# Performance work log

Measured on AMD Instinct MI355X. Metric: run time of the kernel, lower is better.

## Reference

```python
import jax, jax.numpy as jnp
import numpy as np

N = 50000
E = 800000
F_IN = 128
HID = 128
NCLS = 40


def setup_inputs() -> dict:
    key = jax.random.key(0)
    ks = jax.random.split(key, 12)
    def glorot(k, fan_in, fan_out):
        s = jnp.sqrt(6.0 / (fan_in + fan_out))
        return jax.random.uniform(k, (fan_in, fan_out), jnp.float32, -s, s)
    x = jax.random.normal(ks[0], (N, F_IN), jnp.float32)
    edge_index = jax.random.randint(ks[1], (2, E), 0, N, jnp.int64)
    W1 = glorot(ks[2], F_IN, HID); b1 = jnp.zeros((HID,), jnp.float32)
    W2 = glorot(ks[3], HID, HID);  b2 = jnp.zeros((HID,), jnp.float32)
    W3 = glorot(ks[4], HID, HID);  b3 = jnp.zeros((HID,), jnp.float32)
    Wc = glorot(ks[5], HID, NCLS)
    bc = jnp.zeros((NCLS,), jnp.float32)
    return {"x": x, "edge_index": edge_index, "W1": W1, "b1": b1,
            "W2": W2, "b2": b2, "W3": W3, "b3": b3, "Wc": Wc, "bc": bc}


def _gcn_conv(h, src, dst, norm, W, b):
    # GCNConv: linear transform, then normalized scatter-add aggregation
    h = h @ W                              # [N, out]
    msg = h[src] * norm[:, None]           # [E+N, out] gathered + scaled
    out = jax.ops.segment_sum(msg, dst, num_segments=N)
    return out + b


def reference(x, edge_index, W1, b1, W2, b2, W3, b3, Wc, bc):
    # add self-loops (PyG GCNConv default) and compute symmetric norm once
    loop = jnp.arange(N, dtype=edge_index.dtype)
    src = jnp.concatenate([edge_index[0], loop])
    dst = jnp.concatenate([edge_index[1], loop])
    deg = jax.ops.segment_sum(jnp.ones_like(dst, dtype=x.dtype), dst, num_segments=N)
    dinv = jax.lax.rsqrt(deg)              # deg >= 1 due to self-loops
    norm = dinv[src] * dinv[dst]           # [E+N]

    h = jax.nn.relu(_gcn_conv(x, src, dst, norm, W1, b1))
    h = jax.nn.relu(_gcn_conv(h, src, dst, norm, W2, b2))
    h = jax.nn.relu(_gcn_conv(h, src, dst, norm, W3, b3))
    out = h @ Wc + bc
    return (out, h)
```

## Files before the change

### kernel.cpp

```cpp
#include <hip/hip_runtime.h>
#include <hip/hip_fp16.h>


#define FEAT 128

typedef _Float16 half_t;
typedef _Float16 f16x8 __attribute__((ext_vector_type(8)));
typedef float f32x16 __attribute__((ext_vector_type(16)));


__global__ __launch_bounds__(256) void k_prep(const float* __restrict__ W1,
                                              const float* __restrict__ W2,
                                              const float* __restrict__ W3,
                                              half_t* __restrict__ Wt1,
                                              half_t* __restrict__ Wt2,
                                              half_t* __restrict__ Wt3,
                                              int* __restrict__ deg, int N) {
  int idx = blockIdx.x * 256 + threadIdx.x;
  if (idx < N) deg[idx] = 0;
  if (idx < 3 * 16384) {
    int which = idx >> 14;
    int i = idx & 16383;
    int k = i >> 7, n = i & 127;
    const float* W = (which == 0) ? W1 : (which == 1) ? W2 : W3;
    half_t* Wt = (which == 0) ? Wt1 : (which == 1) ? Wt2 : Wt3;
    Wt[n * 128 + k] = (half_t)W[i];
  }
}


__global__ __launch_bounds__(256) void k_count_rank(const int* __restrict__ dst,
                                                    int* __restrict__ deg,
                                                    int* __restrict__ rank, int E) {
  int e = blockIdx.x * 256 + threadIdx.x;
  if (e < E) rank[e] = atomicAdd(&deg[dst[e]], 1);
}

__global__ __launch_bounds__(256) void k_scanA(const int* __restrict__ deg,
                                               int* __restrict__ partial, int N) {
  __shared__ int s[256];
  int t = threadIdx.x;
  int i = blockIdx.x * 256 + t;
  s[t] = (i < N) ? deg[i] : 0;
  __syncthreads();
  for (int off = 128; off > 0; off >>= 1) {
    if (t < off) s[t] += s[t + off];
    __syncthreads();
  }
  if (t == 0) partial[blockIdx.x] = s[0];
}

__global__ __launch_bounds__(256) void k_scanB(int* __restrict__ partial, int nblk,
                                               int* __restrict__ offsets, int N) {
  __shared__ int s[256];
  int t = threadIdx.x;
  int v = (t < nblk) ? partial[t] : 0;
  s[t] = v;
  __syncthreads();
  for (int off = 1; off < 256; off <<= 1) {
    int x = (t >= off) ? s[t - off] : 0;
    __syncthreads();
    s[t] += x;
    __syncthreads();
  }
  if (t < nblk) partial[t] = s[t] - v;
  if (t == 0) offsets[N] = s[255];
}

__global__ __launch_bounds__(256) void k_scanC(const int* __restrict__ deg,
                                               const int* __restrict__ partial,
                                               int* __restrict__ offsets,
                                               float* __restrict__ dinv, int N) {
  __shared__ int s[256];
  int t = threadIdx.x;
  int i = blockIdx.x * 256 + t;
  int v = (i < N) ? deg[i] : 0;
  s[t] = v;
  __syncthreads();
  for (int off = 1; off < 256; off <<= 1) {
    int x = (t >= off) ? s[t - off] : 0;
    __syncthreads();
    s[t] += x;
    __syncthreads();
  }
  if (i < N) {
    offsets[i] = partial[blockIdx.x] + s[t] - v;
    dinv[i] = rsqrtf((float)(v + 1));
  }
}

__global__ __launch_bounds__(256) void k_place(const int* __restrict__ src,
                                               const int* __restrict__ dst,
                                               const int* __restrict__ offsets,
                                               const int* __restrict__ rank,
                                               int* __restrict__ col, int E) {
  int e = blockIdx.x * 256 + threadIdx.x;
  if (e < E) col[offsets[dst[e]] + rank[e]] = src[e];
}

template <int SRC_FP32>
__global__ __launch_bounds__(256) void k_gemm_mfma(const void* __restrict__ Asrc,
                                                   const half_t* __restrict__ Wt,
                                                   const float* __restrict__ dinv,
                                                   half_t* __restrict__ T,
                                                   int nrows) {
  __shared__ char lds[65536];
  char* sA = lds;
  char* sW = lds + 32768;
  int t = threadIdx.x;
  int rowBase = blockIdx.x * 128;
  int rowsHere = min(128, nrows - rowBase);

  #pragma unroll
  for (int i = 0; i < 8; ++i) {
    int lin = t + i * 256;
    int r = lin >> 4, c = lin & 15;
    *(float4*)(sW + r * 256 + ((c * 16) ^ ((r & 15) << 4))) =
        *(const float4*)((const char*)Wt + r * 256 + c * 16);
  }
  if (SRC_FP32) {
    const float* Af = (const float*)Asrc;
    #pragma unroll
    for (int i = 0; i < 8; ++i) {
      int lin = t + i * 256;
      int r = lin >> 4, c = lin & 15;
      f16x8 h = {};
      if (r < rowsHere) {
        const float4* p = (const float4*)(Af + (size_t)(rowBase + r) * FEAT + c * 8);
        float4 v0 = p[0], v1 = p[1];
        h[0] = (half_t)v0.x; h[1] = (half_t)v0.y; h[2] = (half_t)v0.z; h[3] = (half_t)v0.w;
        h[4] = (half_t)v1.x; h[5] = (half_t)v1.y; h[6] = (half_t)v1.z; h[7] = (half_t)v1.w;
      }
      *(f16x8*)(sA + r * 256 + ((c * 16) ^ ((r & 15) << 4))) = h;
    }
  } else {
    const char* Ah = (const char*)Asrc;
    #pragma unroll
    for (int i = 0; i < 8; ++i) {
      int lin = t + i * 256;
      int r = lin >> 4, c = lin & 15;
      float4 v = {};
      if (r < rowsHere) v = *(const float4*)(Ah + (size_t)(rowBase + r) * 256 + c * 16);
      *(float4*)(sA + r * 256 + ((c * 16) ^ ((r & 15) << 4))) = v;
    }
  }
  __syncthreads();

  int wv = t >> 6;
  int l = t & 63;
  int l31 = l & 31;
  int lhi = l >> 5;
  int sw = (l31 & 15) << 4;

  f32x16 acc[4] = {};

  #pragma unroll
  for (int step = 0; step < 8; ++step) {
    int ko = (step * 32 + lhi * 16) ^ sw;
    f16x8 a  = *(const f16x8*)(sA + (wv * 32 + l31) * 256 + ko);
    f16x8 b0 = *(const f16x8*)(sW + (l31) * 256 + ko);
    f16x8 b1 = *(const f16x8*)(sW + (32 + l31) * 256 + ko);
    f16x8 b2 = *(const f16x8*)(sW + (64 + l31) * 256 + ko);
    f16x8 b3 = *(const f16x8*)(sW + (96 + l31) * 256 + ko);
    acc[0] = __builtin_amdgcn_mfma_f32_32x32x16_f16(a, b0, acc[0], 0, 0, 0);
    acc[1] = __builtin_amdgcn_mfma_f32_32x32x16_f16(a, b1, acc[1], 0, 0, 0);
    acc[2] = __builtin_amdgcn_mfma_f32_32x32x16_f16(a, b2, acc[2], 0, 0, 0);
    acc[3] = __builtin_amdgcn_mfma_f32_32x32x16_f16(a, b3, acc[3], 0, 0, 0);
  }

  #pragma unroll
  for (int j = 0; j < 16; ++j) {
    int rloc = wv * 32 + (j & 3) + 8 * (j >> 2) + 4 * lhi;
    if (rloc < rowsHere) {
      int grow = rowBase + rloc;
      float d = dinv[grow];
      #pragma unroll
      for (int n = 0; n < 4; ++n) {
        T[(size_t)grow * FEAT + n * 32 + l31] = (half_t)(acc[n][j] * d);
      }
    }
  }
}

template <int OUTF>
__global__ __launch_bounds__(256) void k_aggregate(const uint2* __restrict__ T4,
                                                   const int* __restrict__ offsets,
                                                   const int* __restrict__ col,
                                                   const float* __restrict__ dinv,
                                                   const float* __restrict__ bias,
                                                   float4* __restrict__ outF,
                                                   uint2* __restrict__ outH,
                                                   int N) {
  int wave = threadIdx.x >> 6;
  int half = (threadIdx.x >> 5) & 1;
  int q = threadIdx.x & 31;
  int node = (blockIdx.x * 4 + wave) * 2 + half;
  if (node >= N) return;
  int e0 = offsets[node], e1 = offsets[node + 1];

  uint2 sv = T4[(size_t)node * 32 + q];
  __half2 h0 = *(__half2*)&sv.x, h1 = *(__half2*)&sv.y;
  float ax = __half2float(h0.x), ay = __half2float(h0.y);
  float az = __half2float(h1.x), aw = __half2float(h1.y);

  int e = e0;
  for (; e + 8 <= e1; e += 8) {
    int s0 = col[e + 0], s1 = col[e + 1], s2 = col[e + 2], s3 = col[e + 3];
    int s4 = col[e + 4], s5 = col[e + 5], s6 = col[e + 6], s7 = col[e + 7];
    uint2 v0 = T4[(size_t)s0 * 32 + q];
    uint2 v1 = T4[(size_t)s1 * 32 + q];
    uint2 v2 = T4[(size_t)s2 * 32 + q];
    uint2 v3 = T4[(size_t)s3 * 32 + q];
    uint2 v4 = T4[(size_t)s4 * 32 + q];
    uint2 v5 = T4[(size_t)s5 * 32 + q];
    uint2 v6 = T4[(size_t)s6 * 32 + q];
    uint2 v7 = T4[(size_t)s7 * 32 + q];
    #pragma unroll
    for (int u = 0; u < 8; ++u) {
      uint2 v = (u == 0) ? v0 : (u == 1) ? v1 : (u == 2) ? v2 : (u == 3) ? v3
              : (u == 4) ? v4 : (u == 5) ? v5 : (u == 6) ? v6 : v7;
      __half2 p0 = *(__half2*)&v.x, p1 = *(__half2*)&v.y;
      ax += __half2float(p0.x); ay += __half2float(p0.y);
      az += __half2float(p1.x); aw += __half2float(p1.y);
    }
  }
  for (; e < e1; ++e) {
    uint2 v = T4[(size_t)col[e] * 32 + q];
    __half2 p0 = *(__half2*)&v.x, p1 = *(__half2*)&v.y;
    ax += __half2float(p0.x); ay += __half2float(p0.y);
    az += __half2float(p1.x); aw += __half2float(p1.y);
  }

  float di = dinv[node];
  float4 b = ((const float4*)bias)[q];
  float ox = fmaxf(di * ax + b.x, 0.f);
  float oy = fmaxf(di * ay + b.y, 0.f);
  float oz = fmaxf(di * az + b.z, 0.f);
  float ow = fmaxf(di * aw + b.w, 0.f);
  if (OUTF) {
    outF[(size_t)node * 32 + q] = make_float4(ox, oy, oz, ow);
  } else {
    uint2 o;
    __half2 t0 = __floats2half2_rn(ox, oy), t1 = __floats2half2_rn(oz, ow);
    o.x = *(unsigned*)&t0; o.y = *(unsigned*)&t1;
    outH[(size_t)node * 32 + q] = o;
  }
}

__global__ __launch_bounds__(256) void k_classifier(const float* __restrict__ h,
                                                    const float* __restrict__ Wc,
                                                    const float* __restrict__ bc,
                                                    float* __restrict__ out, int N) {
  __shared__ float sh[64 * 132];
  __shared__ float sWt[40 * 130];
  int t = threadIdx.x;
  int nodeBase = blockIdx.x * 64;
  int nodesHere = min(64, N - nodeBase);

  for (int i = t; i < FEAT * 40; i += 256) {
    int k = i / 40, c = i - k * 40;
    sWt[c * 130 + k] = Wc[i];
  }
  {
    const float4* H4 = (const float4*)(h + (size_t)nodeBase * FEAT);
    #pragma unroll
    for (int i = 0; i < 8; ++i) {
      int lin = t + i * 256;
      int r = lin >> 5, kc = lin & 31;
      float4 v = make_float4(0.f, 0.f, 0.f, 0.f);
      if (r < nodesHere) v = H4[lin];
      *(float4*)&sh[r * 132 + kc * 4] = v;
    }
  }
  __syncthreads();

  int n0 = (t >> 3) * 2;
  int cg = (t & 7) * 5;
  float acc0[5], acc1[5];
  #pragma unroll
  for (int j = 0; j < 5; ++j) { acc0[j] = bc[cg + j]; acc1[j] = acc0[j]; }

  #pragma unroll 4
  for (int k4 = 0; k4 < 32; ++k4) {
    float4 h0 = *(const float4*)&sh[n0 * 132 + k4 * 4];
    float4 h1 = *(const float4*)&sh[(n0 + 1) * 132 + k4 * 4];
    #pragma unroll
    for (int j = 0; j < 5; ++j) {
      float4 w = *(const float4*)&sWt[(cg + j) * 130 + k4 * 4];
      acc0[j] += h0.x * w.x + h0.y * w.y + h0.z * w.z + h0.w * w.w;
      acc1[j] += h1.x * w.x + h1.y * w.y + h1.z * w.z + h1.w * w.w;
    }
  }

  if (n0 < nodesHere) {
    float* o = out + (size_t)(nodeBase + n0) * 40 + cg;
    #pragma unroll
    for (int j = 0; j < 5; ++j) o[j] = acc0[j];
  }
  if (n0 + 1 < nodesHere) {
    float* o = out + (size_t)(nodeBase + n0 + 1) * 40 + cg;
    #pragma unroll
    for (int j = 0; j < 5; ++j) o[j] = acc1[j];
  }
}


extern "C" void kernel_launch(void* const* d_in, const int* in_sizes, int n_in,
                              void* d_out, int out_size, void* d_ws, size_t ws_size,
                              hipStream_t stream) {
  const float* x    = (const float*)d_in[0];
  const int*   edge = (const int*)d_in[1];
  const float* W1   = (const float*)d_in[2];
  const float* b1   = (const float*)d_in[3];
  const float* W2   = (const float*)d_in[4];
  const float* b2   = (const float*)d_in[5];
  const float* W3   = (const float*)d_in[6];
  const float* b3   = (const float*)d_in[7];
  const float* Wc   = (const float*)d_in[8];
  const float* bc   = (const float*)d_in[9];

  int N = in_sizes[0] / FEAT;
  int E = in_sizes[1] / 2;

  float* out  = (float*)d_out;
  float* hOut = out + (size_t)N * 40;

  size_t o = 0;
  char* wsb = (char*)d_ws;
  auto take = [&](size_t bytes) -> void* {
    void* p = wsb + o;
    o += (bytes + 255) & ~(size_t)255;
    return p;
  };
  float*   dinv    = (float*)take((size_t)N * 4);
  int*     deg     = (int*)take((size_t)N * 4);
  int*     rank    = (int*)take((size_t)E * 4);
  int*     partial = (int*)take(256 * 4);
  int*     offsets = (int*)take(((size_t)N + 8) * 4);
  int*     col     = (int*)take((size_t)E * 4);
  half_t*  T2h     = (half_t*)take((size_t)N * FEAT * 2);
  half_t*  Bh      = (half_t*)take((size_t)N * FEAT * 2);
  half_t*  Wt1     = (half_t*)take(16384 * 2);
  half_t*  Wt2     = (half_t*)take(16384 * 2);
  half_t*  Wt3     = (half_t*)take(16384 * 2);

  const int* e_src = edge;
  const int* e_dst = edge + E;

  int nblk = (N + 255) / 256;
  int eblk = (E + 255) / 256;

  k_prep<<<nblk, 256, 0, stream>>>(W1, W2, W3, Wt1, Wt2, Wt3, deg, N);
  k_count_rank<<<eblk, 256, 0, stream>>>(e_dst, deg, rank, E);
  k_scanA<<<nblk, 256, 0, stream>>>(deg, partial, N);
  k_scanB<<<1, 256, 0, stream>>>(partial, nblk, offsets, N);
  k_scanC<<<nblk, 256, 0, stream>>>(deg, partial, offsets, dinv, N);
  k_place<<<eblk, 256, 0, stream>>>(e_src, e_dst, offsets, rank, col, E);

  int gblk = (N + 127) / 128;
  int ablk = (N + 7) / 8;
  uint2* T4 = (uint2*)T2h;
  k_gemm_mfma<1><<<gblk, 256, 0, stream>>>(x, Wt1, dinv, T2h, N);
  k_aggregate<0><<<ablk, 256, 0, stream>>>(T4, offsets, col, dinv, b1, nullptr,
                                           (uint2*)Bh, N);
  k_gemm_mfma<0><<<gblk, 256, 0, stream>>>(Bh, Wt2, dinv, T2h, N);
  k_aggregate<0><<<ablk, 256, 0, stream>>>(T4, offsets, col, dinv, b2, nullptr,
                                           (uint2*)Bh, N);
  k_gemm_mfma<0><<<gblk, 256, 0, stream>>>(Bh, Wt3, dinv, T2h, N);
  k_aggregate<1><<<ablk, 256, 0, stream>>>(T4, offsets, col, dinv, b3,
                                           (float4*)hOut, nullptr, N);
  k_classifier<<<(N + 63) / 64, 256, 0, stream>>>(hOut, Wc, bc, out, N);
}
```

Measured before the change: 230.3 us.

## Widen aggregate gathers, split GEMM weight staging, fold scan kernels, add nontemporal hints

The aggregation kernel now gives each lane 16-byte fp16 loads (8 features) with 16 lanes per node and 16 nodes per block, up from 8-byte loads and 32 lanes per node. This halves the number of gather instructions and doubles the memory-level parallelism per lane. The GEMM loads the weight tile in two 64-row halves, cutting LDS from 64KB to 48KB to allow higher occupancy, at the cost of an extra barrier. The single-block scan pass is removed: each block now serially sums the preceding partials itself, which is O(nblk) work per block but saves one launch. Nontemporal loads and stores are added to the rank, col, output and intermediate-feature streams.

After: 253.7 us. +10.1%, slower.

```diff
diff --git a/kernel.cpp b/kernel.cpp
--- a/kernel.cpp
+++ b/kernel.cpp
@@ -7,6 +7,7 @@
 typedef _Float16 half_t;
 typedef _Float16 f16x8 __attribute__((ext_vector_type(8)));
 typedef float f32x16 __attribute__((ext_vector_type(16)));
+typedef unsigned int u32x4 __attribute__((ext_vector_type(4)));
 
 
 __global__ __launch_bounds__(256) void k_prep(const float* __restrict__ W1,
@@ -33,7 +34,10 @@
                                                     int* __restrict__ deg,
                                                     int* __restrict__ rank, int E) {
   int e = blockIdx.x * 256 + threadIdx.x;
-  if (e < E) rank[e] = atomicAdd(&deg[dst[e]], 1);
+  if (e < E) {
+    int r = atomicAdd(&deg[dst[e]], 1);
+    __builtin_nontemporal_store(r, &rank[e]);
+  }
 }
 
 __global__ __launch_bounds__(256) void k_scanA(const int* __restrict__ deg,
@@ -50,30 +54,15 @@
   if (t == 0) partial[blockIdx.x] = s[0];
 }
 
-__global__ __launch_bounds__(256) void k_scanB(int* __restrict__ partial, int nblk,
-                                               int* __restrict__ offsets, int N) {
+__global__ __launch_bounds__(256) void k_scanC2(const int* __restrict__ deg,
+                                                const int* __restrict__ partial,
+                                                int* __restrict__ offsets,
+                                                float* __restrict__ dinv, int N) {
   __shared__ int s[256];
   int t = threadIdx.x;
-  int v = (t < nblk) ? partial[t] : 0;
-  s[t] = v;
-  __syncthreads();
-  for (int off = 1; off < 256; off <<= 1) {
-    int x = (t >= off) ? s[t - off] : 0;
-    __syncthreads();
-    s[t] += x;
-    __syncthreads();
-  }
-  if (t < nblk) partial[t] = s[t] - v;
-  if (t == 0) offsets[N] = s[255];
-}
-
-__global__ __launch_bounds__(256) void k_scanC(const int* __restrict__ deg,
-                                               const int* __restrict__ partial,
-                                               int* __restrict__ offsets,
-                                               float* __restrict__ dinv, int N) {
-  __shared__ int s[256];
-  int t = threadIdx.x;
   int i = blockIdx.x * 256 + t;
+  int base = 0;
+  for (int j = 0; j < blockIdx.x; ++j) base += partial[j];
   int v = (i < N) ? deg[i] : 0;
   s[t] = v;
   __syncthreads();
@@ -84,8 +73,9 @@
     __syncthreads();
   }
   if (i < N) {
-    offsets[i] = partial[blockIdx.x] + s[t] - v;
+    offsets[i] = base + s[t] - v;
     dinv[i] = rsqrtf((float)(v + 1));
+    if (i == N - 1) offsets[N] = base + s[t];
   }
 }
 
@@ -95,7 +85,10 @@
                                                const int* __restrict__ rank,
                                                int* __restrict__ col, int E) {
   int e = blockIdx.x * 256 + threadIdx.x;
-  if (e < E) col[offsets[dst[e]] + rank[e]] = src[e];
+  if (e < E) {
+    int r = __builtin_nontemporal_load(&rank[e]);
+    col[offsets[dst[e]] + r] = src[e];
+  }
 }
 
 template <int SRC_FP32>
@@ -104,20 +97,13 @@
                                                    const float* __restrict__ dinv,
                                                    half_t* __restrict__ T,
                                                    int nrows) {
-  __shared__ char lds[65536];
+  __shared__ char lds[49152];
   char* sA = lds;
   char* sW = lds + 32768;
   int t = threadIdx.x;
   int rowBase = blockIdx.x * 128;
   int rowsHere = min(128, nrows - rowBase);
 
-  #pragma unroll
-  for (int i = 0; i < 8; ++i) {
-    int lin = t + i * 256;
-    int r = lin >> 4, c = lin & 15;
-    *(float4*)(sW + r * 256 + ((c * 16) ^ ((r & 15) << 4))) =
-        *(const float4*)((const char*)Wt + r * 256 + c * 16);
-  }
   if (SRC_FP32) {
     const float* Af = (const float*)Asrc;
     #pragma unroll
@@ -144,7 +130,6 @@
       *(float4*)(sA + r * 256 + ((c * 16) ^ ((r & 15) << 4))) = v;
     }
   }
-  __syncthreads();
 
   int wv = t >> 6;
   int l = t & 63;
@@ -155,17 +140,25 @@
   f32x16 acc[4] = {};
 
   #pragma unroll
-  for (int step = 0; step < 8; ++step) {
-    int ko = (step * 32 + lhi * 16) ^ sw;
-    f16x8 a  = *(const f16x8*)(sA + (wv * 32 + l31) * 256 + ko);
-    f16x8 b0 = *(const f16x8*)(sW + (l31) * 256 + ko);
-    f16x8 b1 = *(const f16x8*)(sW + (32 + l31) * 256 + ko);
-    f16x8 b2 = *(const f16x8*)(sW + (64 + l31) * 256 + ko);
-    f16x8 b3 = *(const f16x8*)(sW + (96 + l31) * 256 + ko);
-    acc[0] = __builtin_amdgcn_mfma_f32_32x32x16_f16(a, b0, acc[0], 0, 0, 0);
-    acc[1] = __builtin_amdgcn_mfma_f32_32x32x16_f16(a, b1, acc[1], 0, 0, 0);
-    acc[2] = __builtin_amdgcn_mfma_f32_32x32x16_f16(a, b2, acc[2], 0, 0, 0);
-    acc[3] = __builtin_amdgcn_mfma_f32_32x32x16_f16(a, b3, acc[3], 0, 0, 0);
+  for (int ch = 0; ch < 2; ++ch) {
+    if (ch) __syncthreads();
+    #pragma unroll
+    for (int i = 0; i < 4; ++i) {
+      int lin = t + i * 256;
+      int r = lin >> 4, c = lin & 15;
+      *(float4*)(sW + r * 256 + ((c * 16) ^ ((r & 15) << 4))) =
+          *(const float4*)((const char*)Wt + (ch * 64 + r) * 256 + c * 16);
+    }
+    __syncthreads();
+    #pragma unroll
+    for (int step = 0; step < 8; ++step) {
+      int ko = (step * 32 + lhi * 16) ^ sw;
+      f16x8 a  = *(const f16x8*)(sA + (wv * 32 + l31) * 256 + ko);
+      f16x8 b0 = *(const f16x8*)(sW + (l31) * 256 + ko);
+      f16x8 b1 = *(const f16x8*)(sW + (32 + l31) * 256 + ko);
+      acc[2 * ch + 0] = __builtin_amdgcn_mfma_f32_32x32x16_f16(a, b0, acc[2 * ch + 0], 0, 0, 0);
+      acc[2 * ch + 1] = __builtin_amdgcn_mfma_f32_32x32x16_f16(a, b1, acc[2 * ch + 1], 0, 0, 0);
+    }
   }
 
   #pragma unroll
@@ -182,68 +175,88 @@
   }
 }
 
+
+__device__ __forceinline__ void acc8(float* a, u32x4 v) {
+  unsigned w0 = v[0], w1 = v[1], w2 = v[2], w3 = v[3];
+  __half2 p0 = *(__half2*)&w0, p1 = *(__half2*)&w1;
+  __half2 p2 = *(__half2*)&w2, p3 = *(__half2*)&w3;
+  a[0] += __half2float(p0.x); a[1] += __half2float(p0.y);
+  a[2] += __half2float(p1.x); a[3] += __half2float(p1.y);
+  a[4] += __half2float(p2.x); a[5] += __half2float(p2.y);
+  a[6] += __half2float(p3.x); a[7] += __half2float(p3.y);
+}
+
+__device__ __forceinline__ void gather_node(const u32x4* __restrict__ T8,
+                                            const int* __restrict__ offsets,
+                                            const int* __restrict__ col,
+                                            int node, int q, float* a) {
+  u32x4 sv = T8[(size_t)node * 16 + q];
+  {
+    unsigned w0 = sv[0], w1 = sv[1], w2 = sv[2], w3 = sv[3];
+    __half2 p0 = *(__half2*)&w0, p1 = *(__half2*)&w1;
+    __half2 p2 = *(__half2*)&w2, p3 = *(__half2*)&w3;
+    a[0] = __half2float(p0.x); a[1] = __half2float(p0.y);
+    a[2] = __half2float(p1.x); a[3] = __half2float(p1.y);
+    a[4] = __half2float(p2.x); a[5] = __half2float(p2.y);
+    a[6] = __half2float(p3.x); a[7] = __half2float(p3.y);
+  }
+  int e0 = offsets[node], e1 = offsets[node + 1];
+  int e = e0;
+  for (; e + 8 <= e1; e += 8) {
+    int s[8];
+    u32x4 v[8];
+    #pragma unroll
+    for (int u = 0; u < 8; ++u) s[u] = __builtin_nontemporal_load(&col[e + u]);
+    #pragma unroll
+    for (int u = 0; u < 8; ++u) v[u] = T8[(size_t)s[u] * 16 + q];
+    #pragma unroll
+    for (int u = 0; u < 8; ++u) acc8(a, v[u]);
+  }
+  for (; e < e1; ++e) {
+    int s = __builtin_nontemporal_load(&col[e]);
+    acc8(a, T8[(size_t)s * 16 + q]);
+  }
+}
+
 template <int OUTF>
-__global__ __launch_bounds__(256) void k_aggregate(const uint2* __restrict__ T4,
+__global__ __launch_bounds__(256) void k_aggregate(const u32x4* __restrict__ T8,
                                                    const int* __restrict__ offsets,
                                                    const int* __restrict__ col,
                                                    const float* __restrict__ dinv,
                                                    const float* __restrict__ bias,
+                                                   u32x4* __restrict__ outH,
                                                    float4* __restrict__ outF,
-                                                   uint2* __restrict__ outH,
                                                    int N) {
-  int wave = threadIdx.x >> 6;
-  int half = (threadIdx.x >> 5) & 1;
-  int q = threadIdx.x & 31;
-  int node = (blockIdx.x * 4 + wave) * 2 + half;
+  int t = threadIdx.x;
+  int node = blockIdx.x * 16 + (t >> 4);
+  int q = t & 15;
   if (node >= N) return;
-  int e0 = offsets[node], e1 = offsets[node + 1];
-
-  uint2 sv = T4[(size_t)node * 32 + q];
-  __half2 h0 = *(__half2*)&sv.x, h1 = *(__half2*)&sv.y;
-  float ax = __half2float(h0.x), ay = __half2float(h0.y);
-  float az = __half2float(h1.x), aw = __half2float(h1.y);
-
-  int e = e0;
-  for (; e + 8 <= e1; e += 8) {
-    int s0 = col[e + 0], s1 = col[e + 1], s2 = col[e + 2], s3 = col[e + 3];
-    int s4 = col[e + 4], s5 = col[e + 5], s6 = col[e + 6], s7 = col[e + 7];
-    uint2 v0 = T4[(size_t)s0 * 32 + q];
-    uint2 v1 = T4[(size_t)s1 * 32 + q];
-    uint2 v2 = T4[(size_t)s2 * 32 + q];
-    uint2 v3 = T4[(size_t)s3 * 32 + q];
-    uint2 v4 = T4[(size_t)s4 * 32 + q];
-    uint2 v5 = T4[(size_t)s5 * 32 + q];
-    uint2 v6 = T4[(size_t)s6 * 32 + q];
-    uint2 v7 = T4[(size_t)s7 * 32 + q];
-    #pragma unroll
-    for (int u = 0; u < 8; ++u) {
-      uint2 v = (u == 0) ? v0 : (u == 1) ? v1 : (u == 2) ? v2 : (u == 3) ? v3
-              : (u == 4) ? v4 : (u == 5) ? v5 : (u == 6) ? v6 : v7;
-      __half2 p0 = *(__half2*)&v.x, p1 = *(__half2*)&v.y;
-      ax += __half2float(p0.x); ay += __half2float(p0.y);
-      az += __half2float(p1.x); aw += __half2float(p1.y);
-    }
-  }
-  for (; e < e1; ++e) {
-    uint2 v = T4[(size_t)col[e] * 32 + q];
-    __half2 p0 = *(__half2*)&v.x, p1 = *(__half2*)&v.y;
-    ax += __half2float(p0.x); ay += __half2float(p0.y);
-    az += __half2float(p1.x); aw += __half2float(p1.y);
-  }
+
+  float a[8];
+  gather_node(T8, offsets, col, node, q, a);
 
   float di = dinv[node];
-  float4 b = ((const float4*)bias)[q];
-  float ox = fmaxf(di * ax + b.x, 0.f);
-  float oy = fmaxf(di * ay + b.y, 0.f);
-  float oz = fmaxf(di * az + b.z, 0.f);
-  float ow = fmaxf(di * aw + b.w, 0.f);
+  const float4* b4 = (const float4*)bias;
+  float4 bA = b4[2 * q], bB = b4[2 * q + 1];
+  float o0 = fmaxf(di * a[0] + bA.x, 0.f);
+  float o1 = fmaxf(di * a[1] + bA.y, 0.f);
+  float o2 = fmaxf(di * a[2] + bA.z, 0.f);
+  float o3 = fmaxf(di * a[3] + bA.w, 0.f);
+  float o4 = fmaxf(di * a[4] + bB.x, 0.f);
+  float o5 = fmaxf(di * a[5] + bB.y, 0.f);
+  float o6 = fmaxf(di * a[6] + bB.z, 0.f);
+  float o7 = fmaxf(di * a[7] + bB.w, 0.f);
+
   if (OUTF) {
-    outF[(size_t)node * 32 + q] = make_float4(ox, oy, oz, ow);
+    outF[(size_t)node * 32 + 2 * q] = make_float4(o0, o1, o2, o3);
+    outF[(size_t)node * 32 + 2 * q + 1] = make_float4(o4, o5, o6, o7);
   } else {
-    uint2 o;
-    __half2 t0 = __floats2half2_rn(ox, oy), t1 = __floats2half2_rn(oz, ow);
-    o.x = *(unsigned*)&t0; o.y = *(unsigned*)&t1;
-    outH[(size_t)node * 32 + q] = o;
+    __half2 h0 = __floats2half2_rn(o0, o1), h1 = __floats2half2_rn(o2, o3);
+    __half2 h2 = __floats2half2_rn(o4, o5), h3 = __floats2half2_rn(o6, o7);
+    u32x4 o;
+    o[0] = *(unsigned*)&h0; o[1] = *(unsigned*)&h1;
+    o[2] = *(unsigned*)&h2; o[3] = *(unsigned*)&h3;
+    __builtin_nontemporal_store(o, &outH[(size_t)node * 16 + q]);
   }
 }
 
@@ -295,12 +308,12 @@
   if (n0 < nodesHere) {
     float* o = out + (size_t)(nodeBase + n0) * 40 + cg;
     #pragma unroll
-    for (int j = 0; j < 5; ++j) o[j] = acc0[j];
+    for (int j = 0; j < 5; ++j) __builtin_nontemporal_store(acc0[j], &o[j]);
   }
   if (n0 + 1 < nodesHere) {
     float* o = out + (size_t)(nodeBase + n0 + 1) * 40 + cg;
     #pragma unroll
-    for (int j = 0; j < 5; ++j) o[j] = acc1[j];
+    for (int j = 0; j < 5; ++j) __builtin_nontemporal_store(acc1[j], &o[j]);
   }
 }
 
@@ -353,21 +366,20 @@
   k_prep<<<nblk, 256, 0, stream>>>(W1, W2, W3, Wt1, Wt2, Wt3, deg, N);
   k_count_rank<<<eblk, 256, 0, stream>>>(e_dst, deg, rank, E);
   k_scanA<<<nblk, 256, 0, stream>>>(deg, partial, N);
-  k_scanB<<<1, 256, 0, stream>>>(partial, nblk, offsets, N);
-  k_scanC<<<nblk, 256, 0, stream>>>(deg, partial, offsets, dinv, N);
+  k_scanC2<<<nblk, 256, 0, stream>>>(deg, partial, offsets, dinv, N);
   k_place<<<eblk, 256, 0, stream>>>(e_src, e_dst, offsets, rank, col, E);
 
   int gblk = (N + 127) / 128;
-  int ablk = (N + 7) / 8;
-  uint2* T4 = (uint2*)T2h;
+  int ablk = (N + 15) / 16;
+  u32x4* T8 = (u32x4*)T2h;
   k_gemm_mfma<1><<<gblk, 256, 0, stream>>>(x, Wt1, dinv, T2h, N);
-  k_aggregate<0><<<ablk, 256, 0, stream>>>(T4, offsets, col, dinv, b1, nullptr,
-                                           (uint2*)Bh, N);
+  k_aggregate<0><<<ablk, 256, 0, stream>>>(T8, offsets, col, dinv, b1,
+                                           (u32x4*)Bh, nullptr, N);
   k_gemm_mfma<0><<<gblk, 256, 0, stream>>>(Bh, Wt2, dinv, T2h, N);
-  k_aggregate<0><<<ablk, 256, 0, stream>>>(T4, offsets, col, dinv, b2, nullptr,
-                                           (uint2*)Bh, N);
+  k_aggregate<0><<<ablk, 256, 0, stream>>>(T8, offsets, col, dinv, b2,
+                                           (u32x4*)Bh, nullptr, N);
   k_gemm_mfma<0><<<gblk, 256, 0, stream>>>(Bh, Wt3, dinv, T2h, N);
-  k_aggregate<1><<<ablk, 256, 0, stream>>>(T4, offsets, col, dinv, b3,
-                                           (float4*)hOut, nullptr, N);
+  k_aggregate<1><<<ablk, 256, 0, stream>>>(T8, offsets, col, dinv, b3,
+                                           nullptr, (float4*)hOut, N);
   k_classifier<<<(N + 63) / 64, 256, 0, stream>>>(hOut, Wc, bc, out, N);
 }
```
